# Performance work log

Hardware: AMD Instinct MI355X
Metric: run time of the kernel (lower is better)

Reference implementation:

```python
import jax, jax.numpy as jnp
import numpy as np

B, S, DIM = 8, 1024, 192
D2 = 2 * DIM            # inner width 384
CH = 4                  # cell heads (= qk_size)
HD = D2 // CH           # 96 head dim
NB = D2 // 4            # 96 block-diagonal blocks
BLK = D2 // NB          # block size 4
TAU = float(HD) ** 0.5


def setup_inputs() -> dict:
    key = jax.random.key(0)
    ks = jax.random.split(key, 16)
    r = lambda i, shp, s=0.02: jax.random.normal(ks[i], shp, jnp.float32) * s
    return {
        "x": jax.random.normal(ks[0], (B, S, DIM), jnp.float32),
        "ln_g": jnp.ones((DIM,), jnp.float32), "ln_b": jnp.zeros((DIM,), jnp.float32),
        "w1": r(1, (D2, DIM)), "b1": jnp.zeros((D2,), jnp.float32),
        "w2": r(2, (D2, DIM)), "b2": jnp.zeros((D2,), jnp.float32),
        "conv_w": r(3, (D2, 1, 3), 0.1), "conv_b": jnp.zeros((D2,), jnp.float32),
        "qw": r(4, (NB, BLK, BLK), 0.1), "qb": jnp.zeros((D2,), jnp.float32),
        "kw": r(5, (NB, BLK, BLK), 0.1), "kb": jnp.zeros((D2,), jnp.float32),
        "vw": r(6, (NB, BLK, BLK), 0.1), "vb": jnp.zeros((D2,), jnp.float32),
        "wi": r(7, (CH, 3 * D2)), "bi": jax.random.normal(ks[8], (CH,), jnp.float32) * 0.1,
        "wf": r(9, (CH, 3 * D2)), "bf": jnp.linspace(3.0, 6.0, CH).astype(jnp.float32),
        "gn_g": jnp.ones((D2,), jnp.float32), "gn_b": jnp.zeros((D2,), jnp.float32),
        "wo": r(10, (DIM, D2)), "bo": jnp.zeros((DIM,), jnp.float32),
        "skip": jnp.ones((D2,), jnp.float32),
    }


def _layernorm(x, g, b):
    m = x.mean(-1, keepdims=True)
    v = ((x - m) ** 2).mean(-1, keepdims=True)
    return (x - m) / jnp.sqrt(v + 1e-5) * g + b


def _blockdiag(x, w, b):
    # x: [B,S,D2] -> blocks [B,S,NB,BLK]; w: [NB, out_blk, in_blk]
    bs, sq, _ = x.shape
    y = jnp.einsum('bsni,noi->bsno', x.reshape(bs, sq, NB, BLK), w)
    return y.reshape(bs, sq, D2) + b


def _dwconv(x, w, b):
    # depthwise conv over sequence: x [B,S,C] -> [B,C,S] conv -> [B,S,C]
    y = jax.lax.conv_general_dilated(
        x.transpose(0, 2, 1), w, window_strides=(1,), padding=[(1, 1)],
        dimension_numbers=('NCH', 'OIH', 'NCH'), feature_group_count=D2)
    return y.transpose(0, 2, 1) + b


def _cell(q, k, v, wi, bi, wf, bf, gn_g, gn_b):
    bs, sq, _ = q.shape
    gi = jnp.concatenate([q, k, v], axis=-1)                      # [B,S,3*D2]
    it = jnp.einsum('bsc,hc->bhs', gi, wi) + bi[None, :, None]    # [B,H,S]
    ft = jnp.einsum('bsc,hc->bhs', gi, wf) + bf[None, :, None]
    c = jnp.cumsum(jax.nn.log_sigmoid(ft), axis=-1)               # [B,H,S]
    logm = c[..., :, None] - c[..., None, :]                      # cum[i]-cum[j]
    mask = jnp.tril(jnp.ones((sq, sq), dtype=bool))
    f_act = jnp.where(mask, logm, -jnp.inf)
    dt = f_act + it[:, :, None, :]                                # add itilde over cols
    max_d = jnp.max(dt, axis=-1, keepdims=True)
    dmat = jnp.exp(dt - max_d)                                    # [B,H,S,S]
    qh = q.reshape(bs, sq, CH, HD).transpose(0, 2, 1, 3)
    kh = k.reshape(bs, sq, CH, HD).transpose(0, 2, 1, 3)
    vh = v.reshape(bs, sq, CH, HD).transpose(0, 2, 1, 3)
    ct = jnp.einsum('bhid,bhjd->bhij', qh, kh) * dmat / TAU
    maxit = jnp.maximum(jnp.abs(ct.sum(-1, keepdims=True)), jnp.exp(-max_d))
    h = jnp.einsum('bhij,bhjd->bhid', ct, vh) / (maxit + 1e-6)
    h = h.transpose(0, 2, 1, 3).reshape(bs, sq, CH, HD)           # per-token GroupNorm
    mu = h.mean(-1, keepdims=True)
    var = ((h - mu) ** 2).mean(-1, keepdims=True)
    h = (h - mu) / jnp.sqrt(var + 1e-5)
    h = h * gn_g.reshape(CH, HD) + gn_b.reshape(CH, HD)
    return h.reshape(bs, sq, D2)


def reference(x, ln_g, ln_b, w1, b1, w2, b2, conv_w, conv_b, qw, qb, kw, kb,
              vw, vb, wi, bi, wf, bf, gn_g, gn_b, wo, bo, skip):
    inputs = _layernorm(x, ln_g, ln_b)
    a = inputs @ w1.T + b1                   # [B,S,D2]
    bgate = jax.nn.silu(inputs @ w2.T + b2)  # [B,S,D2]
    qk = jax.nn.silu(_dwconv(a, conv_w, conv_b))
    q = _blockdiag(qk, qw, qb)
    k = _blockdiag(qk, kw, kb)
    v = _blockdiag(a, vw, vb)
    out1 = _cell(q, k, v, wi, bi, wf, bf, gn_g, gn_b)
    out1 = (out1 + skip * qk) * bgate
    out = out1 @ wo.T + bo
    return out + x
```

## Files before the change

### kernel.cpp

```cpp
#include <hip/hip_runtime.h>
#include <cstdint>

#define TAU_ 9.797958971132712f

typedef __attribute__((ext_vector_type(4))) float f32x4;
typedef __attribute__((ext_vector_type(8))) short short8;

#define DEV static __device__ __forceinline__

DEV unsigned short f2bf(float f){
  union { float f; unsigned u; } v; v.f = f;
  unsigned r = v.u + 0x7FFFu + ((v.u >> 16) & 1u);
  return (unsigned short)(r >> 16);
}
DEV float bf2f(unsigned short u){
  union { unsigned u; float f; } v; v.u = ((unsigned)u) << 16; return v.f;
}
DEV unsigned pack2bf(float a, float b){
  unsigned r;
  asm("v_cvt_pk_bf16_f32 %0, %1, %2" : "=v"(r) : "v"(a), "v"(b));
  return r;
}
DEV float siluf_(float x){ return x / (1.f + __expf(-x)); }
DEV float logsigf_(float x){ return fminf(x, 0.f) - log1pf(__expf(-fabsf(x))); }

__global__ __launch_bounds__(256) void k1b_gemm(
    const float* __restrict__ x, const float* __restrict__ ln_g, const float* __restrict__ ln_b,
    const float* __restrict__ w1, const float* __restrict__ w2,
    const float* __restrict__ b1, const float* __restrict__ b2,
    float* __restrict__ a, unsigned short* __restrict__ bgate)
{
  __shared__ short xn[64][200];
  __shared__ short wt[18432];
  const int tid = threadIdx.x;
  const int ntg = blockIdx.x & 7;
  const int t0 = (blockIdx.x >> 3) * 64;
  {
    const int row = tid >> 2, g = tid & 3;
    const float* xr = x + (long)(t0 + row) * 192 + g * 48;
    float xv[48];
    float s = 0.f, sq = 0.f;
    #pragma unroll
    for(int i = 0; i < 12; i++){
      f32x4 v = *(const f32x4*)(xr + i * 4);
      xv[i*4+0]=v[0]; xv[i*4+1]=v[1]; xv[i*4+2]=v[2]; xv[i*4+3]=v[3];
      s  += v[0]+v[1]+v[2]+v[3];
      sq += v[0]*v[0]+v[1]*v[1]+v[2]*v[2]+v[3]*v[3];
    }
    s  += __shfl_xor(s, 1);  s  += __shfl_xor(s, 2);
    sq += __shfl_xor(sq, 1); sq += __shfl_xor(sq, 2);
    const float mean = s * (1.f/192.f);
    const float rstd = rsqrtf(sq * (1.f/192.f) - mean * mean + 1e-5f);
    unsigned* xrow = (unsigned*)&xn[row][0];
    #pragma unroll
    for(int i = 0; i < 48; i += 2){
      const int c = g * 48 + i;
      float v0 = (xv[i]   - mean) * rstd * ln_g[c]   + ln_b[c];
      float v1 = (xv[i+1] - mean) * rstd * ln_g[c+1] + ln_b[c+1];
      xrow[c >> 1] = pack2bf(v0, v1);
    }
  }
  {
    const float* src = (ntg < 4 ? w1 : w2) + (long)(ntg & 3) * 96 * 192;
    #pragma unroll
    for(int i = 0; i < 9; i++){
      const int u = i * 256 + tid;
      const int row = u / 24;
      const int dst = (u * 16) ^ ((row & 7) << 4);
      f32x4 f0 = *(const f32x4*)(src + u * 8);
      f32x4 f1 = *(const f32x4*)(src + u * 8 + 4);
      uint4 pk;
      pk.x = pack2bf(f0[0], f0[1]); pk.y = pack2bf(f0[2], f0[3]);
      pk.z = pack2bf(f1[0], f1[1]); pk.w = pack2bf(f1[2], f1[3]);
      *(uint4*)((char*)wt + dst) = pk;
    }
  }
  __syncthreads();
  const int widx = tid >> 6, lane = tid & 63, qg = lane >> 4, l16 = lane & 15;
  const int mrow = widx * 16 + l16;
  f32x4 acc[6];
  #pragma unroll
  for(int nt = 0; nt < 6; nt++) acc[nt] = (f32x4){0.f,0.f,0.f,0.f};
  #pragma unroll
  for(int kc = 0; kc < 6; kc++){
    short8 af = *(const short8*)(&xn[mrow][0] + kc * 32 + 8 * qg);
    #pragma unroll
    for(int nt = 0; nt < 6; nt++){
      const int row = nt * 16 + l16;
      int byte = row * 384 + (kc * 32 + 8 * qg) * 2;
      byte ^= (row & 7) << 4;
      short8 bfr = *(const short8*)((const char*)wt + byte);
      acc[nt] = __builtin_amdgcn_mfma_f32_16x16x32_bf16(af, bfr, acc[nt], 0, 0, 0);
    }
  }
  const int half = ntg >> 2;
  const float* bias = half ? b2 : b1;
  const int ncol = (ntg & 3) * 96;
  #pragma unroll
  for(int nt = 0; nt < 6; nt++){
    const int n = ncol + nt * 16 + l16;
    const float bs = bias[n];
    #pragma unroll
    for(int r = 0; r < 4; r++){
      const int trow = t0 + widx * 16 + 4 * qg + r;
      float v = acc[nt][r] + bs;
      if(half) bgate[(long)trow * 384 + n] = f2bf(siluf_(v));
      else     a[(long)trow * 384 + n] = v;
    }
  }
}

__global__ __launch_bounds__(256) void k2bv(
    const float* __restrict__ a, const float* __restrict__ cw, const float* __restrict__ cb,
    const float* __restrict__ qw, const float* __restrict__ qb,
    const float* __restrict__ kw, const float* __restrict__ kb,
    const float* __restrict__ vw, const float* __restrict__ vb,
    float* __restrict__ qkbuf, short* __restrict__ qbf, short* __restrict__ kbf,
    short* __restrict__ vtbf)
{
  __shared__ float vt[64][97];
  const int tid = threadIdx.x;
  const int bh = blockIdx.x >> 4;
  const int b = bh >> 2, h = bh & 3;
  const int s0 = (blockIdx.x & 15) << 6;
  #pragma unroll
  for(int it = 0; it < 6; it++){
    const int f = it * 256 + tid;
    const int sl = f / 24, c4l = f % 24;
    const int c4 = h * 24 + c4l;
    const int s = s0 + sl;
    const long t = (long)b * 1024 + s;
    const long abase = t * 384 + c4 * 4;
    f32x4 am = *(const f32x4*)(a + abase);
    f32x4 al = (s > 0)    ? *(const f32x4*)(a + abase - 384) : (f32x4){0.f,0.f,0.f,0.f};
    f32x4 ar = (s < 1023) ? *(const f32x4*)(a + abase + 384) : (f32x4){0.f,0.f,0.f,0.f};
    f32x4 cw0 = *(const f32x4*)(cw + c4 * 12);
    f32x4 cw1 = *(const f32x4*)(cw + c4 * 12 + 4);
    f32x4 cw2 = *(const f32x4*)(cw + c4 * 12 + 8);
    f32x4 cb4 = *(const f32x4*)(cb + c4 * 4);
    f32x4 in;
    in[0] = siluf_(cb4[0] + al[0]*cw0[0] + am[0]*cw0[1] + ar[0]*cw0[2]);
    in[1] = siluf_(cb4[1] + al[1]*cw0[3] + am[1]*cw1[0] + ar[1]*cw1[1]);
    in[2] = siluf_(cb4[2] + al[2]*cw1[2] + am[2]*cw1[3] + ar[2]*cw2[0]);
    in[3] = siluf_(cb4[3] + al[3]*cw2[1] + am[3]*cw2[2] + ar[3]*cw2[3]);
    *(f32x4*)(qkbuf + abase) = in;
    const long base = ((long)(b * 4 + h) * 1024 + s) * 96 + c4l * 4;
    {
      const float* w = qw + c4 * 16;
      float v0 = qb[c4*4+0] + w[0]*in[0]  + w[1]*in[1]  + w[2]*in[2]  + w[3]*in[3];
      float v1 = qb[c4*4+1] + w[4]*in[0]  + w[5]*in[1]  + w[6]*in[2]  + w[7]*in[3];
      float v2 = qb[c4*4+2] + w[8]*in[0]  + w[9]*in[1]  + w[10]*in[2] + w[11]*in[3];
      float v3 = qb[c4*4+3] + w[12]*in[0] + w[13]*in[1] + w[14]*in[2] + w[15]*in[3];
      uint2 pk; pk.x = pack2bf(v0, v1); pk.y = pack2bf(v2, v3);
      *(uint2*)(qbf + base) = pk;
    }
    {
      const float* w = kw + c4 * 16;
      float v0 = kb[c4*4+0] + w[0]*in[0]  + w[1]*in[1]  + w[2]*in[2]  + w[3]*in[3];
      float v1 = kb[c4*4+1] + w[4]*in[0]  + w[5]*in[1]  + w[6]*in[2]  + w[7]*in[3];
      float v2 = kb[c4*4+2] + w[8]*in[0]  + w[9]*in[1]  + w[10]*in[2] + w[11]*in[3];
      float v3 = kb[c4*4+3] + w[12]*in[0] + w[13]*in[1] + w[14]*in[2] + w[15]*in[3];
      uint2 pk; pk.x = pack2bf(v0, v1); pk.y = pack2bf(v2, v3);
      *(uint2*)(kbf + base) = pk;
    }
    {
      const float* w = vw + c4 * 16;
      #pragma unroll
      for(int o = 0; o < 4; o++){
        float v = vb[c4*4+o] + w[o*4]*am[0] + w[o*4+1]*am[1] + w[o*4+2]*am[2] + w[o*4+3]*am[3];
        vt[sl][c4l * 4 + o] = v;
      }
    }
  }
  __syncthreads();
  #pragma unroll
  for(int it = 0; it < 24; it++){
    const int f = it * 256 + tid;
    const int d = f >> 6, sl = f & 63;
    vtbf[((long)bh * 96 + d) * 1024 + s0 + sl] = (short)f2bf(vt[sl][d]);
  }
}

__global__ __launch_bounds__(256) void k2c_gates(
    const short* __restrict__ qbf, const short* __restrict__ kbf,
    const float* __restrict__ a,
    const float* __restrict__ vw, const float* __restrict__ vb,
    const float* __restrict__ wi, const float* __restrict__ bi,
    const float* __restrict__ wf, const float* __restrict__ bff,
    float* __restrict__ itv, float* __restrict__ ftv)
{
  const int tid = threadIdx.x;
  const int lane = tid & 63, widx = tid >> 6;
  const int t = blockIdx.x * 4 + widx;
  const int b = t >> 10, s = t & 1023;
  float pit[4] = {0,0,0,0}, pft[4] = {0,0,0,0};
  for(int j = 0; j < 18; j++){
    const int e = lane + 64 * j;
    float val;
    if(e < 768){
      const int c = (e >= 384) ? e - 384 : e;
      const short* src = (e >= 384) ? kbf : qbf;
      const int h = c / 96, d = c - h * 96;
      val = bf2f((unsigned short)src[((long)(b * 4 + h) * 1024 + s) * 96 + d]);
    } else {
      const int c = e - 768;
      const int c4 = c >> 2, o = c & 3;
      f32x4 in = *(const f32x4*)(a + (long)t * 384 + c4 * 4);
      const float* w = vw + c4 * 16 + o * 4;
      val = vb[c] + w[0]*in[0] + w[1]*in[1] + w[2]*in[2] + w[3]*in[3];
    }
    #pragma unroll
    for(int h = 0; h < 4; h++){
      pit[h] += val * wi[h * 1152 + e];
      pft[h] += val * wf[h * 1152 + e];
    }
  }
  #pragma unroll
  for(int h = 0; h < 4; h++){
    float vi = pit[h], vf = pft[h];
    #pragma unroll
    for(int m = 1; m < 64; m <<= 1){ vi += __shfl_xor(vi, m); vf += __shfl_xor(vf, m); }
    if(lane == 0){
      itv[((long)(b * 4 + h)) * 1024 + s] = vi + bi[h];
      ftv[((long)(b * 4 + h)) * 1024 + s] = vf + bff[h];
    }
  }
}

__global__ __launch_bounds__(256) void k3_scan(
    const float* __restrict__ itv, const float* __restrict__ ftv,
    float* __restrict__ Ev, float* __restrict__ Rpv, float* __restrict__ dsv)
{
  __shared__ float sb[256];
  const int bh = blockIdx.x, tid = threadIdx.x;
  const long base = (long)bh * 1024 + tid * 4;
  f32x4 f4 = *(const f32x4*)(ftv + base);
  const float l0 = logsigf_(f4[0]);
  const float l1 = logsigf_(f4[1]);
  const float l2 = logsigf_(f4[2]);
  const float l3 = logsigf_(f4[3]);
  float c0 = l0, c1 = l0 + l1, c2 = c1 + l2, c3 = c2 + l3;
  sb[tid] = c3;
  __syncthreads();
  for(int off = 1; off < 256; off <<= 1){
    float mine = sb[tid];
    float oth = (tid >= off) ? sb[tid - off] : 0.f;
    __syncthreads();
    sb[tid] = mine + oth;
    __syncthreads();
  }
  const float excl = (tid > 0) ? sb[tid - 1] : 0.f;
  c0 += excl; c1 += excl; c2 += excl; c3 += excl;
  f32x4 i4 = *(const f32x4*)(itv + base);
  const float m0 = i4[0] - c0, m1 = i4[1] - c1, m2 = i4[2] - c2, m3 = i4[3] - c3;
  const float x1 = fmaxf(m0, m1), x2 = fmaxf(x1, m2), x3 = fmaxf(x2, m3);
  __syncthreads();
  sb[tid] = x3;
  __syncthreads();
  for(int off = 1; off < 256; off <<= 1){
    float mine = sb[tid];
    float oth = (tid >= off) ? sb[tid - off] : -3.4e38f;
    __syncthreads();
    sb[tid] = fmaxf(mine, oth);
    __syncthreads();
  }
  const float exm = (tid > 0) ? sb[tid - 1] : -3.4e38f;
  const float M0 = fmaxf(m0, exm);
  const float M1 = fmaxf(x1, exm);
  const float M2 = fmaxf(x2, exm);
  const float M3 = fmaxf(x3, exm);
  f32x4 e, rp, ds;
  e[0] = __expf(m0); e[1] = __expf(m1); e[2] = __expf(m2); e[3] = __expf(m3);
  rp[0] = __expf(-M0) * (1.f/TAU_); rp[1] = __expf(-M1) * (1.f/TAU_);
  rp[2] = __expf(-M2) * (1.f/TAU_); rp[3] = __expf(-M3) * (1.f/TAU_);
  ds[0] = __expf(-(c0 + M0)); ds[1] = __expf(-(c1 + M1));
  ds[2] = __expf(-(c2 + M2)); ds[3] = __expf(-(c3 + M3));
  *(f32x4*)(Ev  + base) = e;
  *(f32x4*)(Rpv + base) = rp;
  *(f32x4*)(dsv + base) = ds;
}

__global__ __launch_bounds__(256, 2) void k4_attn(
    const short* __restrict__ qbf, const short* __restrict__ kbf, const short* __restrict__ vtbf,
    const float* __restrict__ Ev, const float* __restrict__ Rpv, const float* __restrict__ dsv,
    const float* __restrict__ gn_g, const float* __restrict__ gn_b,
    const float* __restrict__ qk, const unsigned short* __restrict__ bgate,
    const float* __restrict__ skip, short* __restrict__ o1bf)
{
  __shared__ short kbuf[2][64 * 104];
  __shared__ short vbuf[2][96 * 72];
  __shared__ float ebuf[2][64];
  __shared__ short P[4][16][72];
  const int tid = threadIdx.x;
  const int w = tid >> 6, lane = tid & 63, qg = lane >> 4, l16 = lane & 15;
  const int xcd = blockIdx.x & 7, q = blockIdx.x >> 3;
  const int bh = ((q & 3) << 3) | xcd;
  const int qh = q >> 2;
  const int ib = (q < 32) ? (15 - qh) : (qh - 8);
  const int i0w = ib * 64 + w * 16;
  const long qkbase = (long)bh * 1024;
  const int nj = ib + 1;

  short8 qf[3];
  #pragma unroll
  for(int kc = 0; kc < 3; kc++)
    qf[kc] = *(const short8*)(qbf + (qkbase + i0w + l16) * 96 + kc * 32 + 8 * qg);
  const float rp = Rpv[qkbase + i0w + l16];
  const float ds = dsv[qkbase + i0w + l16];

  f32x4 acc[6];
  #pragma unroll
  for(int dt = 0; dt < 6; dt++) acc[dt] = (f32x4){0.f,0.f,0.f,0.f};
  float bp = 0.f;

  const int rK0 = tid / 12,        cK0 = tid % 12;
  const int rK1 = (tid+256) / 12,  cK1 = (tid+256) % 12;
  const int rK2 = (tid+512) / 12,  cK2 = (tid+512) % 12;
  const int dV0 = tid >> 3,        cV0 = tid & 7;
  const int dV1 = (tid+256) >> 3,  cV1 = (tid+256) & 7;
  const int dV2 = (tid+512) >> 3,  cV2 = (tid+512) & 7;
  const bool he = (tid < 16);
  short8 sk0, sk1, sk2, sv0, sv1, sv2; f32x4 se;
  const short* kgb = kbf + qkbase * 96;
  const short* vgb = vtbf + (long)bh * 96 * 1024;

#define STAGE_LOAD(J0)                                              \
  {                                                                 \
    const int j0_ = (J0);                                           \
    sk0 = *(const short8*)(kgb + (j0_ + rK0) * 96 + cK0 * 8);       \
    sk1 = *(const short8*)(kgb + (j0_ + rK1) * 96 + cK1 * 8);       \
    sk2 = *(const short8*)(kgb + (j0_ + rK2) * 96 + cK2 * 8);       \
    sv0 = *(const short8*)(vgb + (long)dV0 * 1024 + j0_ + cV0 * 8); \
    sv1 = *(const short8*)(vgb + (long)dV1 * 1024 + j0_ + cV1 * 8); \
    sv2 = *(const short8*)(vgb + (long)dV2 * 1024 + j0_ + cV2 * 8); \
    if(he) se = *(const f32x4*)(Ev + qkbase + j0_ + tid * 4);       \
  }

#define STAGE_WRITE(B)                                   \
  {                                                      \
    *(short8*)(&kbuf[B][rK0 * 104 + cK0 * 8]) = sk0;     \
    *(short8*)(&kbuf[B][rK1 * 104 + cK1 * 8]) = sk1;     \
    *(short8*)(&kbuf[B][rK2 * 104 + cK2 * 8]) = sk2;     \
    *(short8*)(&vbuf[B][dV0 * 72 + cV0 * 8]) = sv0;      \
    *(short8*)(&vbuf[B][dV1 * 72 + cV1 * 8]) = sv1;      \
    *(short8*)(&vbuf[B][dV2 * 72 + cV2 * 8]) = sv2;      \
    if(he) *(f32x4*)(&ebuf[B][tid * 4]) = se;            \
  }

  STAGE_LOAD(0);
  int cur = 0;
  for(int jt = 0; jt < nj; jt++){
    STAGE_WRITE(cur);
    __syncthreads();
    if(jt + 1 < nj) STAGE_LOAD((jt + 1) * 64);

    const int j0 = jt * 64;
    const bool diag = (jt == nj - 1);
    const int i = i0w + l16;
    __builtin_amdgcn_s_setprio(1);
    #pragma unroll
    for(int jsub = 0; jsub < 4; jsub++){
      f32x4 C = (f32x4){0.f,0.f,0.f,0.f};
      #pragma unroll
      for(int kc = 0; kc < 3; kc++){
        short8 kf = *(const short8*)(&kbuf[cur][(jsub*16 + l16) * 104 + kc * 32 + 8 * qg]);
        C = __builtin_amdgcn_mfma_f32_16x16x32_bf16(kf, qf[kc], C, 0, 0, 0);
      }
      f32x4 e4 = *(const f32x4*)(&ebuf[cur][jsub * 16 + 4 * qg]);
      float v0 = C[0] * e4[0];
      float v1 = C[1] * e4[1];
      float v2 = C[2] * e4[2];
      float v3 = C[3] * e4[3];
      if(diag){
        const int jb = j0 + jsub * 16 + 4 * qg;
        if(jb + 0 > i) v0 = 0.f;
        if(jb + 1 > i) v1 = 0.f;
        if(jb + 2 > i) v2 = 0.f;
        if(jb + 3 > i) v3 = 0.f;
      }
      bp += v0 + v1 + v2 + v3;
      uint2 pw; pw.x = pack2bf(v0, v1); pw.y = pack2bf(v2, v3);
      *(uint2*)(&P[w][l16][jsub * 16 + 4 * qg]) = pw;
    }
    asm volatile("s_waitcnt lgkmcnt(0)" ::: "memory");
    #pragma unroll
    for(int ksub = 0; ksub < 2; ksub++){
      short8 pa = *(const short8*)(&P[w][l16][ksub * 32 + 8 * qg]);
      #pragma unroll
      for(int dt = 0; dt < 6; dt++){
        short8 vf = *(const short8*)(&vbuf[cur][(dt * 16 + l16) * 72 + ksub * 32 + 8 * qg]);
        acc[dt] = __builtin_amdgcn_mfma_f32_16x16x32_bf16(pa, vf, acc[dt], 0, 0, 0);
      }
    }
    __builtin_amdgcn_s_setprio(0);
    cur ^= 1;
  }
#undef STAGE_LOAD
#undef STAGE_WRITE

  const int head = bh & 3, bb = bh >> 2;
  float bsum = bp;
  bsum += __shfl_xor(bsum, 16);
  bsum += __shfl_xor(bsum, 32);
  const float bfull = bsum * rp;
  const float den = fmaxf(fabsf(bfull), ds) + 1e-6f;
  const float sc = rp / den;
  float srow[4];
  #pragma unroll
  for(int r = 0; r < 4; r++) srow[r] = __shfl(sc, 4 * qg + r);
  float hv[6][4], mu[4], rs[4];
  #pragma unroll
  for(int r = 0; r < 4; r++){
    float sm = 0.f, sq = 0.f;
    #pragma unroll
    for(int dt = 0; dt < 6; dt++){
      const float h = acc[dt][r] * srow[r];
      hv[dt][r] = h; sm += h; sq += h * h;
    }
    sm += __shfl_xor(sm, 1); sm += __shfl_xor(sm, 2); sm += __shfl_xor(sm, 4); sm += __shfl_xor(sm, 8);
    sq += __shfl_xor(sq, 1); sq += __shfl_xor(sq, 2); sq += __shfl_xor(sq, 4); sq += __shfl_xor(sq, 8);
    const float m_ = sm * (1.f/96.f);
    mu[r] = m_;
    rs[r] = rsqrtf(sq * (1.f/96.f) - m_ * m_ + 1e-5f);
  }
  #pragma unroll
  for(int dt = 0; dt < 6; dt++){
    const int col = head * 96 + dt * 16 + l16;
    const float g  = gn_g[col];
    const float be = gn_b[col];
    const float sk = skip[col];
    #pragma unroll
    for(int r = 0; r < 4; r++){
      const long off = ((long)(bb * 1024 + i0w + 4 * qg + r)) * 384 + col;
      const float hn = (hv[dt][r] - mu[r]) * rs[r] * g + be;
      const float o1 = (hn + sk * qk[off]) * bf2f(bgate[off]);
      o1bf[off] = (short)f2bf(o1);
    }
  }
}

__global__ __launch_bounds__(256) void k5_gemm(
    const short* __restrict__ o1bf, const float* __restrict__ wo,
    const float* __restrict__ bo, const float* __restrict__ x, float* __restrict__ out)
{
  __shared__ short wt[18432];
  const int tid = threadIdx.x;
  const int ng = blockIdx.x & 3;
  const int t0 = (blockIdx.x >> 2) * 64;
  {
    const float* src = wo + (long)ng * 48 * 384;
    #pragma unroll
    for(int i = 0; i < 9; i++){
      const int u = i * 256 + tid;
      const int row = u / 48;
      const int dst = (u * 16) ^ ((row & 7) << 4);
      f32x4 f0 = *(const f32x4*)(src + u * 8);
      f32x4 f1 = *(const f32x4*)(src + u * 8 + 4);
      uint4 pk;
      pk.x = pack2bf(f0[0], f0[1]); pk.y = pack2bf(f0[2], f0[3]);
      pk.z = pack2bf(f1[0], f1[1]); pk.w = pack2bf(f1[2], f1[3]);
      *(uint4*)((char*)wt + dst) = pk;
    }
  }
  __syncthreads();
  const int widx = tid >> 6, lane = tid & 63, qg = lane >> 4, l16 = lane & 15;
  f32x4 acc[3];
  #pragma unroll
  for(int nt = 0; nt < 3; nt++) acc[nt] = (f32x4){0.f,0.f,0.f,0.f};
  const short* arow = o1bf + (long)(t0 + widx * 16 + l16) * 384;
  #pragma unroll
  for(int kc = 0; kc < 12; kc++){
    short8 af = *(const short8*)(arow + kc * 32 + 8 * qg);
    #pragma unroll
    for(int nt = 0; nt < 3; nt++){
      const int row = nt * 16 + l16;
      int byte = row * 768 + kc * 64 + qg * 16;
      byte ^= (row & 7) << 4;
      short8 bfr = *(const short8*)((const char*)wt + byte);
      acc[nt] = __builtin_amdgcn_mfma_f32_16x16x32_bf16(af, bfr, acc[nt], 0, 0, 0);
    }
  }
  #pragma unroll
  for(int nt = 0; nt < 3; nt++){
    const int n = ng * 48 + nt * 16 + l16;
    const float b_ = bo[n];
    #pragma unroll
    for(int r = 0; r < 4; r++){
      const int trow = t0 + widx * 16 + 4 * qg + r;
      out[(long)trow * 192 + n] = acc[nt][r] + b_ + x[(long)trow * 192 + n];
    }
  }
}

extern "C" void kernel_launch(void* const* d_in, const int* in_sizes, int n_in,
                              void* d_out, int out_size, void* d_ws, size_t ws_size,
                              hipStream_t stream)
{
  (void)in_sizes; (void)n_in; (void)out_size; (void)ws_size;
  const float* x    = (const float*)d_in[0];
  const float* ln_g = (const float*)d_in[1];
  const float* ln_b = (const float*)d_in[2];
  const float* w1   = (const float*)d_in[3];
  const float* b1   = (const float*)d_in[4];
  const float* w2   = (const float*)d_in[5];
  const float* b2   = (const float*)d_in[6];
  const float* cw   = (const float*)d_in[7];
  const float* cb   = (const float*)d_in[8];
  const float* qw   = (const float*)d_in[9];
  const float* qb   = (const float*)d_in[10];
  const float* kw   = (const float*)d_in[11];
  const float* kb   = (const float*)d_in[12];
  const float* vw   = (const float*)d_in[13];
  const float* vb   = (const float*)d_in[14];
  const float* wi   = (const float*)d_in[15];
  const float* bi   = (const float*)d_in[16];
  const float* wf   = (const float*)d_in[17];
  const float* bff  = (const float*)d_in[18];
  const float* gn_g = (const float*)d_in[19];
  const float* gn_b = (const float*)d_in[20];
  const float* wo   = (const float*)d_in[21];
  const float* bo   = (const float*)d_in[22];
  const float* skip = (const float*)d_in[23];
  float* out = (float*)d_out;

  char* ws = (char*)d_ws;
  float* a_    = (float*)(ws + 0);
  unsigned short* bgate = (unsigned short*)(ws + 12582912);
  float* qkbuf = (float*)(ws + 25165824);
  short* o1bf  = (short*)(ws + 41943040);
  short* qbf   = (short*)(ws + 50331648);
  short* kbf   = (short*)(ws + 56623104);
  short* vtbf  = (short*)(ws + 62914560);
  float* itv   = (float*)(ws + 69648384);
  float* ftv   = (float*)(ws + 69779456);
  float* Ev    = (float*)(ws + 69910528);
  float* Rpv   = (float*)(ws + 70041600);
  float* dsv   = (float*)(ws + 70172672);

  k1b_gemm<<<1024, 256, 0, stream>>>(x, ln_g, ln_b, w1, w2, b1, b2, a_, bgate);
  k2bv<<<512, 256, 0, stream>>>(a_, cw, cb, qw, qb, kw, kb, vw, vb, qkbuf, qbf, kbf, vtbf);
  k2c_gates<<<2048, 256, 0, stream>>>(qbf, kbf, a_, vw, vb, wi, bi, wf, bff, itv, ftv);
  k3_scan<<<32, 256, 0, stream>>>(itv, ftv, Ev, Rpv, dsv);
  k4_attn<<<512, 256, 0, stream>>>(qbf, kbf, vtbf, Ev, Rpv, dsv, gn_g, gn_b,
                                   qkbuf, bgate, skip, o1bf);
  k5_gemm<<<512, 256, 0, stream>>>(o1bf, wo, bo, x, out);
}
```

Before: 92.36 us.

## Split LayerNorm into its own kernel and store intermediates a/qk in bf16

LayerNorm now runs once per token in a separate kernel that writes a bf16 normalized input. Before, each of the 8 column-group blocks of the GEMM recomputed it. The GEMM reads A fragments straight from global memory. The intermediates a and qk are now stored as bf16 instead of fp32, which halves their write and read traffic in the conv/blockdiag, gates and attention epilogue kernels. The cost is an extra kernel launch plus an extra round trip for xn, and reduced precision on v, the conv input and the skip term.

```diff
diff --git a/kernel.cpp b/kernel.cpp
--- a/kernel.cpp
+++ b/kernel.cpp
@@ -21,45 +21,64 @@
   asm("v_cvt_pk_bf16_f32 %0, %1, %2" : "=v"(r) : "v"(a), "v"(b));
   return r;
 }
+DEV f32x4 ld_bf4(const unsigned short* p){
+  uint2 r = *(const uint2*)p;
+  f32x4 o;
+  o[0] = bf2f((unsigned short)(r.x & 0xffff));
+  o[1] = bf2f((unsigned short)(r.x >> 16));
+  o[2] = bf2f((unsigned short)(r.y & 0xffff));
+  o[3] = bf2f((unsigned short)(r.y >> 16));
+  return o;
+}
 DEV float siluf_(float x){ return x / (1.f + __expf(-x)); }
 DEV float logsigf_(float x){ return fminf(x, 0.f) - log1pf(__expf(-fabsf(x))); }
 
+__global__ __launch_bounds__(256) void k1a_ln(
+    const float* __restrict__ x, const float* __restrict__ ln_g, const float* __restrict__ ln_b,
+    short* __restrict__ xnbf)
+{
+  const int tid = threadIdx.x;
+  const int t = blockIdx.x * 16 + (tid >> 4);
+  const int g = tid & 15;
+  const float* xr = x + (long)t * 192 + g * 12;
+  f32x4 v0 = *(const f32x4*)(xr);
+  f32x4 v1 = *(const f32x4*)(xr + 4);
+  f32x4 v2 = *(const f32x4*)(xr + 8);
+  float s  = v0[0]+v0[1]+v0[2]+v0[3] + v1[0]+v1[1]+v1[2]+v1[3] + v2[0]+v2[1]+v2[2]+v2[3];
+  float sq = v0[0]*v0[0]+v0[1]*v0[1]+v0[2]*v0[2]+v0[3]*v0[3]
+           + v1[0]*v1[0]+v1[1]*v1[1]+v1[2]*v1[2]+v1[3]*v1[3]
+           + v2[0]*v2[0]+v2[1]*v2[1]+v2[2]*v2[2]+v2[3]*v2[3];
+  s  += __shfl_xor(s, 1);  s  += __shfl_xor(s, 2);  s  += __shfl_xor(s, 4);  s  += __shfl_xor(s, 8);
+  sq += __shfl_xor(sq, 1); sq += __shfl_xor(sq, 2); sq += __shfl_xor(sq, 4); sq += __shfl_xor(sq, 8);
+  const float mean = s * (1.f/192.f);
+  const float rstd = rsqrtf(sq * (1.f/192.f) - mean * mean + 1e-5f);
+  const int c0 = g * 12;
+  f32x4 g0 = *(const f32x4*)(ln_g + c0),     b0 = *(const f32x4*)(ln_b + c0);
+  f32x4 g1 = *(const f32x4*)(ln_g + c0 + 4), b1 = *(const f32x4*)(ln_b + c0 + 4);
+  f32x4 g2 = *(const f32x4*)(ln_g + c0 + 8), b2 = *(const f32x4*)(ln_b + c0 + 8);
+  unsigned pk[6];
+  pk[0] = pack2bf((v0[0]-mean)*rstd*g0[0]+b0[0], (v0[1]-mean)*rstd*g0[1]+b0[1]);
+  pk[1] = pack2bf((v0[2]-mean)*rstd*g0[2]+b0[2], (v0[3]-mean)*rstd*g0[3]+b0[3]);
+  pk[2] = pack2bf((v1[0]-mean)*rstd*g1[0]+b1[0], (v1[1]-mean)*rstd*g1[1]+b1[1]);
+  pk[3] = pack2bf((v1[2]-mean)*rstd*g1[2]+b1[2], (v1[3]-mean)*rstd*g1[3]+b1[3]);
+  pk[4] = pack2bf((v2[0]-mean)*rstd*g2[0]+b2[0], (v2[1]-mean)*rstd*g2[1]+b2[1]);
+  pk[5] = pack2bf((v2[2]-mean)*rstd*g2[2]+b2[2], (v2[3]-mean)*rstd*g2[3]+b2[3]);
+  uint2* xo = (uint2*)(xnbf + (long)t * 192 + g * 12);
+  xo[0] = make_uint2(pk[0], pk[1]);
+  xo[1] = make_uint2(pk[2], pk[3]);
+  xo[2] = make_uint2(pk[4], pk[5]);
+}
+
 __global__ __launch_bounds__(256) void k1b_gemm(
-    const float* __restrict__ x, const float* __restrict__ ln_g, const float* __restrict__ ln_b,
+    const short* __restrict__ xnbf,
     const float* __restrict__ w1, const float* __restrict__ w2,
     const float* __restrict__ b1, const float* __restrict__ b2,
-    float* __restrict__ a, unsigned short* __restrict__ bgate)
-{
-  __shared__ short xn[64][200];
+    unsigned short* __restrict__ abf, unsigned short* __restrict__ bgate)
+{
   __shared__ short wt[18432];
   const int tid = threadIdx.x;
   const int ntg = blockIdx.x & 7;
   const int t0 = (blockIdx.x >> 3) * 64;
-  {
-    const int row = tid >> 2, g = tid & 3;
-    const float* xr = x + (long)(t0 + row) * 192 + g * 48;
-    float xv[48];
-    float s = 0.f, sq = 0.f;
-    #pragma unroll
-    for(int i = 0; i < 12; i++){
-      f32x4 v = *(const f32x4*)(xr + i * 4);
-      xv[i*4+0]=v[0]; xv[i*4+1]=v[1]; xv[i*4+2]=v[2]; xv[i*4+3]=v[3];
-      s  += v[0]+v[1]+v[2]+v[3];
-      sq += v[0]*v[0]+v[1]*v[1]+v[2]*v[2]+v[3]*v[3];
-    }
-    s  += __shfl_xor(s, 1);  s  += __shfl_xor(s, 2);
-    sq += __shfl_xor(sq, 1); sq += __shfl_xor(sq, 2);
-    const float mean = s * (1.f/192.f);
-    const float rstd = rsqrtf(sq * (1.f/192.f) - mean * mean + 1e-5f);
-    unsigned* xrow = (unsigned*)&xn[row][0];
-    #pragma unroll
-    for(int i = 0; i < 48; i += 2){
-      const int c = g * 48 + i;
-      float v0 = (xv[i]   - mean) * rstd * ln_g[c]   + ln_b[c];
-      float v1 = (xv[i+1] - mean) * rstd * ln_g[c+1] + ln_b[c+1];
-      xrow[c >> 1] = pack2bf(v0, v1);
-    }
-  }
   {
     const float* src = (ntg < 4 ? w1 : w2) + (long)(ntg & 3) * 96 * 192;
     #pragma unroll
@@ -81,9 +100,10 @@
   f32x4 acc[6];
   #pragma unroll
   for(int nt = 0; nt < 6; nt++) acc[nt] = (f32x4){0.f,0.f,0.f,0.f};
+  const short* xrow = xnbf + (long)(t0 + mrow) * 192;
   #pragma unroll
   for(int kc = 0; kc < 6; kc++){
-    short8 af = *(const short8*)(&xn[mrow][0] + kc * 32 + 8 * qg);
+    short8 af = *(const short8*)(xrow + kc * 32 + 8 * qg);
     #pragma unroll
     for(int nt = 0; nt < 6; nt++){
       const int row = nt * 16 + l16;
@@ -105,17 +125,18 @@
       const int trow = t0 + widx * 16 + 4 * qg + r;
       float v = acc[nt][r] + bs;
       if(half) bgate[(long)trow * 384 + n] = f2bf(siluf_(v));
-      else     a[(long)trow * 384 + n] = v;
+      else     abf[(long)trow * 384 + n] = f2bf(v);
     }
   }
 }
 
 __global__ __launch_bounds__(256) void k2bv(
-    const float* __restrict__ a, const float* __restrict__ cw, const float* __restrict__ cb,
+    const unsigned short* __restrict__ abf,
+    const float* __restrict__ cw, const float* __restrict__ cb,
     const float* __restrict__ qw, const float* __restrict__ qb,
     const float* __restrict__ kw, const float* __restrict__ kb,
     const float* __restrict__ vw, const float* __restrict__ vb,
-    float* __restrict__ qkbuf, short* __restrict__ qbf, short* __restrict__ kbf,
+    unsigned short* __restrict__ qkbf, short* __restrict__ qbf, short* __restrict__ kbf,
     short* __restrict__ vtbf)
 {
   __shared__ float vt[64][97];
@@ -131,9 +152,9 @@
     const int s = s0 + sl;
     const long t = (long)b * 1024 + s;
     const long abase = t * 384 + c4 * 4;
-    f32x4 am = *(const f32x4*)(a + abase);
-    f32x4 al = (s > 0)    ? *(const f32x4*)(a + abase - 384) : (f32x4){0.f,0.f,0.f,0.f};
-    f32x4 ar = (s < 1023) ? *(const f32x4*)(a + abase + 384) : (f32x4){0.f,0.f,0.f,0.f};
+    f32x4 am = ld_bf4(abf + abase);
+    f32x4 al = (s > 0)    ? ld_bf4(abf + abase - 384) : (f32x4){0.f,0.f,0.f,0.f};
+    f32x4 ar = (s < 1023) ? ld_bf4(abf + abase + 384) : (f32x4){0.f,0.f,0.f,0.f};
     f32x4 cw0 = *(const f32x4*)(cw + c4 * 12);
     f32x4 cw1 = *(const f32x4*)(cw + c4 * 12 + 4);
     f32x4 cw2 = *(const f32x4*)(cw + c4 * 12 + 8);
@@ -143,7 +164,10 @@
     in[1] = siluf_(cb4[1] + al[1]*cw0[3] + am[1]*cw1[0] + ar[1]*cw1[1]);
     in[2] = siluf_(cb4[2] + al[2]*cw1[2] + am[2]*cw1[3] + ar[2]*cw2[0]);
     in[3] = siluf_(cb4[3] + al[3]*cw2[1] + am[3]*cw2[2] + ar[3]*cw2[3]);
-    *(f32x4*)(qkbuf + abase) = in;
+    {
+      uint2 pk; pk.x = pack2bf(in[0], in[1]); pk.y = pack2bf(in[2], in[3]);
+      *(uint2*)(qkbf + abase) = pk;
+    }
     const long base = ((long)(b * 4 + h) * 1024 + s) * 96 + c4l * 4;
     {
       const float* w = qw + c4 * 16;
@@ -183,7 +207,7 @@
 
 __global__ __launch_bounds__(256) void k2c_gates(
     const short* __restrict__ qbf, const short* __restrict__ kbf,
-    const float* __restrict__ a,
+    const unsigned short* __restrict__ abf,
     const float* __restrict__ vw, const float* __restrict__ vb,
     const float* __restrict__ wi, const float* __restrict__ bi,
     const float* __restrict__ wf, const float* __restrict__ bff,
@@ -205,7 +229,7 @@
     } else {
       const int c = e - 768;
       const int c4 = c >> 2, o = c & 3;
-      f32x4 in = *(const f32x4*)(a + (long)t * 384 + c4 * 4);
+      f32x4 in = ld_bf4(abf + (long)t * 384 + c4 * 4);
       const float* w = vw + c4 * 16 + o * 4;
       val = vb[c] + w[0]*in[0] + w[1]*in[1] + w[2]*in[2] + w[3]*in[3];
     }
@@ -284,7 +308,7 @@
     const short* __restrict__ qbf, const short* __restrict__ kbf, const short* __restrict__ vtbf,
     const float* __restrict__ Ev, const float* __restrict__ Rpv, const float* __restrict__ dsv,
     const float* __restrict__ gn_g, const float* __restrict__ gn_b,
-    const float* __restrict__ qk, const unsigned short* __restrict__ bgate,
+    const unsigned short* __restrict__ qkbf, const unsigned short* __restrict__ bgate,
     const float* __restrict__ skip, short* __restrict__ o1bf)
 {
   __shared__ short kbuf[2][64 * 104];
@@ -433,7 +457,7 @@
     for(int r = 0; r < 4; r++){
       const long off = ((long)(bb * 1024 + i0w + 4 * qg + r)) * 384 + col;
       const float hn = (hv[dt][r] - mu[r]) * rs[r] * g + be;
-      const float o1 = (hn + sk * qk[off]) * bf2f(bgate[off]);
+      const float o1 = (hn + sk * bf2f(qkbf[off])) * bf2f(bgate[off]);
       o1bf[off] = (short)f2bf(o1);
     }
   }
@@ -524,9 +548,10 @@
   float* out = (float*)d_out;
 
   char* ws = (char*)d_ws;
-  float* a_    = (float*)(ws + 0);
+  unsigned short* abf   = (unsigned short*)(ws + 0);
   unsigned short* bgate = (unsigned short*)(ws + 12582912);
-  float* qkbuf = (float*)(ws + 25165824);
+  unsigned short* qkbf  = (unsigned short*)(ws + 25165824);
+  short* xnbf  = (short*)(ws + 37748736);
   short* o1bf  = (short*)(ws + 41943040);
   short* qbf   = (short*)(ws + 50331648);
   short* kbf   = (short*)(ws + 56623104);
@@ -537,11 +562,12 @@
   float* Rpv   = (float*)(ws + 70041600);
   float* dsv   = (float*)(ws + 70172672);
 
-  k1b_gemm<<<1024, 256, 0, stream>>>(x, ln_g, ln_b, w1, w2, b1, b2, a_, bgate);
-  k2bv<<<512, 256, 0, stream>>>(a_, cw, cb, qw, qb, kw, kb, vw, vb, qkbuf, qbf, kbf, vtbf);
-  k2c_gates<<<2048, 256, 0, stream>>>(qbf, kbf, a_, vw, vb, wi, bi, wf, bff, itv, ftv);
+  k1a_ln<<<512, 256, 0, stream>>>(x, ln_g, ln_b, xnbf);
+  k1b_gemm<<<1024, 256, 0, stream>>>(xnbf, w1, w2, b1, b2, abf, bgate);
+  k2bv<<<512, 256, 0, stream>>>(abf, cw, cb, qw, qb, kw, kb, vw, vb, qkbf, qbf, kbf, vtbf);
+  k2c_gates<<<2048, 256, 0, stream>>>(qbf, kbf, abf, vw, vb, wi, bi, wf, bff, itv, ftv);
   k3_scan<<<32, 256, 0, stream>>>(itv, ftv, Ev, Rpv, dsv);
   k4_attn<<<512, 256, 0, stream>>>(qbf, kbf, vtbf, Ev, Rpv, dsv, gn_g, gn_b,
-                                   qkbuf, bgate, skip, o1bf);
+                                   qkbf, bgate, skip, o1bf);
   k5_gemm<<<512, 256, 0, stream>>>(o1bf, wo, bo, x, out);
 }
```

New measurement: 88.91 us. 1.04x faster.
